# Optimization experiments

Hardware: AMD Instinct MI355X
Metric: run time of the kernel (lower is better)

The kernel has to match this reference:

```python
import jax, jax.numpy as jnp
import numpy as np

N_NODES = 50000
N_EDGES = 800000
IN_DIM = 128
HIDDEN = 64
NEG_SLOPE = 0.2


def setup_inputs() -> dict:
    key = jax.random.key(0)
    ks = jax.random.split(key, 8)
    x = jax.random.normal(ks[0], (N_NODES, IN_DIM), dtype=jnp.float32)
    edge_index = jax.random.randint(ks[1], (2, N_EDGES), 0, N_NODES, dtype=jnp.int64)
    # GATConv params (heads=1)
    W = jax.random.normal(ks[2], (HIDDEN, IN_DIM), dtype=jnp.float32) / np.sqrt(IN_DIM)
    att_src = jax.random.normal(ks[3], (HIDDEN,), dtype=jnp.float32) / np.sqrt(HIDDEN)
    att_dst = jax.random.normal(ks[4], (HIDDEN,), dtype=jnp.float32) / np.sqrt(HIDDEN)
    bias_conv = jnp.zeros((HIDDEN,), dtype=jnp.float32)
    # final Linear(hidden, 1)
    W_lin = jax.random.normal(ks[5], (1, HIDDEN), dtype=jnp.float32) / np.sqrt(HIDDEN)
    b_lin = jnp.zeros((1,), dtype=jnp.float32)
    return {"x": x, "edge_index": edge_index, "W": W, "att_src": att_src,
            "att_dst": att_dst, "bias_conv": bias_conv, "W_lin": W_lin, "b_lin": b_lin}


def _gat_forward(x, edge_index, W, att_src, att_dst, bias_conv, W_lin, b_lin):
    n = x.shape[0]
    # add self-loops (PyG GATConv default)
    loop = jnp.arange(n, dtype=edge_index.dtype)
    src = jnp.concatenate([edge_index[0], loop])  # source nodes j (messages from)
    dst = jnp.concatenate([edge_index[1], loop])  # destination nodes i (aggregated at)

    h = x @ W.T                                   # [N, H] projected features
    a_src = h @ att_src                           # [N]
    a_dst = h @ att_dst                           # [N]

    e = jax.nn.leaky_relu(a_src[src] + a_dst[dst], NEG_SLOPE)  # [E']
    # segment softmax over incoming edges of each destination node
    m = jax.ops.segment_max(e, dst, num_segments=n)            # [N]
    ex = jnp.exp(e - m[dst])
    s = jax.ops.segment_sum(ex, dst, num_segments=n)           # [N]
    alpha = ex / s[dst]                                        # [E']

    out = jax.ops.segment_sum(alpha[:, None] * h[src], dst, num_segments=n)
    out = out + bias_conv                         # [N, H]

    out = jax.nn.relu(out)
    # dropout p=0.5 is a no-op in eval mode
    y = jax.nn.sigmoid(out @ W_lin.T + b_lin)     # [N, 1]
    return y


def reference(x, edge_index, W, att_src, att_dst, bias_conv, W_lin, b_lin):
    return _gat_forward(x, edge_index, W, att_src, att_dst, bias_conv, W_lin, b_lin)
```

## Files before the change

### kernel.cpp

```cpp
#include <hip/hip_runtime.h>
#include <hip/hip_bf16.h>
#include <hip/hip_fp16.h>
#include <cstdint>

#define IND 128
#define HID 64
#define NEG_SLOPE 0.2f
#define EPB 4096
#define CBSHIFT 8
#define BCAP 8192
#define SORT_THREADS 256
#define EPT (EPB / SORT_THREADS)
#define QCAP 2048
#define GT 512
#define GSCAN (BCAP / GT)

__device__ __forceinline__ unsigned short f2bf_bits(float f) {
  __hip_bfloat16 b = __float2bfloat16(f);
  return *reinterpret_cast<unsigned short*>(&b);
}
__device__ __forceinline__ unsigned short f2h_bits(float f) {
  __half h = __float2half(f);
  return *reinterpret_cast<unsigned short*>(&h);
}
__device__ __forceinline__ float h2f_bits(unsigned short u) {
  __half_raw r; r.x = u;
  return __half2float(__half(r));
}
__device__ __forceinline__ float bf2f_bits(unsigned short u) {
  return __uint_as_float((unsigned)u << 16);
}
__device__ __forceinline__ unsigned pack_bf2(float lo, float hi) {
  return (unsigned)f2bf_bits(lo) | ((unsigned)f2bf_bits(hi) << 16);
}
__device__ __forceinline__ float bf_lo(unsigned u) {
  return __uint_as_float(u << 16);
}
__device__ __forceinline__ float bf_hi(unsigned u) {
  return __uint_as_float(u & 0xFFFF0000u);
}

__global__ __launch_bounds__(256) void k_proj_sort(
    const float* __restrict__ x, const float* __restrict__ W,
    const float* __restrict__ att_s, const float* __restrict__ att_d,
    unsigned short* __restrict__ h, float* __restrict__ a_src,
    float* __restrict__ a_dst,
    const int* __restrict__ ei, int* __restrict__ gcur,
    unsigned* __restrict__ tmp, int E, long long E2,
    int nSort, int nbuck, int n)
{
  __shared__ __align__(16) char smem[49664];
  const int tid = threadIdx.x;

  if (blockIdx.x < (unsigned)nSort) {
    int* hist       = (int*)smem;
    int* sums       = hist + 256;
    int* cur        = sums + 256;
    int* gbase      = cur + 256;
    unsigned* sorted = (unsigned*)(gbase + 256);

    hist[tid] = 0;
    __syncthreads();

    const long long i0 = (long long)blockIdx.x * EPB;

    unsigned pk[EPT];
#pragma unroll
    for (int j = 0; j < EPT; ++j) {
      long long idx = i0 + j * SORT_THREADS + tid;
      unsigned v = 0xFFFFFFFFu;
      if (idx < E2) {
        int s, d;
        if (idx < E) { s = ei[idx]; d = ei[E + idx]; }
        else         { s = d = (int)(idx - E); }
        v = ((unsigned)d << 16) | (unsigned)s;
        atomicAdd(&hist[d >> CBSHIFT], 1);
      }
      pk[j] = v;
    }
    __syncthreads();

    sums[tid] = hist[tid];
    __syncthreads();
    for (int off = 1; off < 256; off <<= 1) {
      int t = (tid >= off) ? sums[tid - off] : 0;
      __syncthreads();
      sums[tid] += t;
      __syncthreads();
    }
    {
      const int lstart_t = sums[tid] - hist[tid];
      cur[tid] = lstart_t;
      gbase[tid] = (tid < nbuck && hist[tid] > 0)
                     ? tid * BCAP + atomicAdd(&gcur[tid], hist[tid]) : 0;
    }
    __syncthreads();
    hist[tid] = sums[tid] - hist[tid];
    __syncthreads();

#pragma unroll
    for (int j = 0; j < EPT; ++j) {
      unsigned v = pk[j];
      if (v != 0xFFFFFFFFu) {
        int b = v >> (16 + CBSHIFT);
        int lpos = atomicAdd(&cur[b], 1);
        sorted[lpos] = v;
      }
    }
    __syncthreads();

    const int cntE = (int)((E2 - i0 < EPB) ? (E2 - i0) : EPB);
    for (int i = tid; i < cntE; i += SORT_THREADS) {
      unsigned v = sorted[i];
      int b = v >> (16 + CBSHIFT);
      tmp[gbase[b] + (i - hist[b])] = v;
    }
    return;
  }

  float*    xs   = (float*)smem;
  unsigned* wt   = (unsigned*)(smem + 32768);
  float*    sa_l = (float*)(smem + 49152);
  float*    sd_l = (float*)(smem + 49408);

  const int nodeBase = (blockIdx.x - nSort) * 64;

  if (tid < 64) { sa_l[tid] = 0.f; sd_l[tid] = 0.f; }

#pragma unroll
  for (int it = 0; it < 4; ++it) {
    int fi = (it * 256 + tid) * 8;
    int row = fi >> 7, k = fi & 127;
    float4 w0 = *(const float4*)(W + fi);
    float4 w1 = *(const float4*)(W + fi + 4);
    uint4 pv;
    pv.x = pack_bf2(w0.x, w0.y);
    pv.y = pack_bf2(w0.z, w0.w);
    pv.z = pack_bf2(w1.x, w1.y);
    pv.w = pack_bf2(w1.z, w1.w);
    int c = (k >> 3) ^ ((row >> 2) & 7);
    ((uint4*)wt)[row * 16 + c] = pv;
  }
#pragma unroll
  for (int it = 0; it < 8; ++it) {
    int fi = (it * 256 + tid) * 4;
    int nl = fi >> 7, k = fi & 127;
    int ks = k ^ (((nl >> 2) & 7) << 2);
    int node = nodeBase + nl; if (node >= n) node = n - 1;
    float4 v = *(const float4*)(x + (size_t)node * IND + k);
    *(float4*)&xs[nl * 128 + ks] = v;
  }
  __syncthreads();

  const int ng = tid & 15;
  const int hg = tid >> 4;
  const int swzA = (ng & 7) << 2;
  const int swzB = hg & 7;
  const float* xrow0 = &xs[(4 * ng) * 128];
  const uint4* wrow0 = ((const uint4*)wt) + (4 * hg) * 16;

  float acc[4][4];
#pragma unroll
  for (int j = 0; j < 4; ++j)
#pragma unroll
    for (int i = 0; i < 4; ++i) acc[j][i] = 0.f;

  for (int k = 0; k < IND; k += 8) {
    float4 a0[4], a1[4];
#pragma unroll
    for (int j = 0; j < 4; ++j) {
      a0[j] = *(const float4*)(xrow0 + j * 128 + (k ^ swzA));
      a1[j] = *(const float4*)(xrow0 + j * 128 + ((k + 4) ^ swzA));
    }
    uint4 bw[4];
#pragma unroll
    for (int i = 0; i < 4; ++i)
      bw[i] = wrow0[i * 16 + ((k >> 3) ^ swzB)];

#pragma unroll
    for (int i = 0; i < 4; ++i) {
      float b0 = bf_lo(bw[i].x), b1 = bf_hi(bw[i].x);
      float b2 = bf_lo(bw[i].y), b3 = bf_hi(bw[i].y);
      float b4 = bf_lo(bw[i].z), b5 = bf_hi(bw[i].z);
      float b6 = bf_lo(bw[i].w), b7 = bf_hi(bw[i].w);
#pragma unroll
      for (int j = 0; j < 4; ++j) {
        acc[j][i] = fmaf(a0[j].x, b0, acc[j][i]);
        acc[j][i] = fmaf(a0[j].y, b1, acc[j][i]);
        acc[j][i] = fmaf(a0[j].z, b2, acc[j][i]);
        acc[j][i] = fmaf(a0[j].w, b3, acc[j][i]);
        acc[j][i] = fmaf(a1[j].x, b4, acc[j][i]);
        acc[j][i] = fmaf(a1[j].y, b5, acc[j][i]);
        acc[j][i] = fmaf(a1[j].z, b6, acc[j][i]);
        acc[j][i] = fmaf(a1[j].w, b7, acc[j][i]);
      }
    }
  }

#pragma unroll
  for (int j = 0; j < 4; ++j) {
    int node = nodeBase + 4 * ng + j;
    if (node < n) {
      ushort4 hv;
      hv.x = f2bf_bits(acc[j][0]);
      hv.y = f2bf_bits(acc[j][1]);
      hv.z = f2bf_bits(acc[j][2]);
      hv.w = f2bf_bits(acc[j][3]);
      *(ushort4*)(h + (size_t)node * HID + 4 * hg) = hv;
    }
  }

  float4 as4 = *(const float4*)(att_s + 4 * hg);
  float4 ad4 = *(const float4*)(att_d + 4 * hg);
#pragma unroll
  for (int j = 0; j < 4; ++j) {
    float ps = acc[j][0]*as4.x + acc[j][1]*as4.y + acc[j][2]*as4.z + acc[j][3]*as4.w;
    float pd = acc[j][0]*ad4.x + acc[j][1]*ad4.y + acc[j][2]*ad4.z + acc[j][3]*ad4.w;
    ps += __shfl_xor(ps, 16, 64); ps += __shfl_xor(ps, 32, 64);
    pd += __shfl_xor(pd, 16, 64); pd += __shfl_xor(pd, 32, 64);
    if ((tid & 63) < 16) {
      atomicAdd(&sa_l[4 * ng + j], ps);
      atomicAdd(&sd_l[4 * ng + j], pd);
    }
  }
  __syncthreads();
  if (tid < 64) {
    int node = nodeBase + tid;
    if (node < n) { a_src[node] = sa_l[tid]; a_dst[node] = sd_l[tid]; }
  }
}

__global__ __launch_bounds__(GT) void k_csr_gather(
    const unsigned* __restrict__ tmp, const int* __restrict__ gcur,
    const float* __restrict__ a_src, const float* __restrict__ a_dst,
    const unsigned short* __restrict__ h,
    const float* __restrict__ bias, const float* __restrict__ W_lin,
    const float* __restrict__ b_lin, float* __restrict__ y, int n)
{
  __shared__ int degl[64], sums[64], cur[64];
  __shared__ float adl[64];
  __shared__ unsigned csrw[QCAP];

  const int tid  = threadIdx.x;
  const int blk  = blockIdx.x;
  const int b    = blk >> 2;
  const int n0   = (b << CBSHIFT) + ((blk & 3) << 6);
  const int base = b * BCAP;
  const int next = base + gcur[b];

  if (tid < 64) {
    degl[tid] = 0;
    const int node = n0 + tid;
    adl[tid] = (node < n) ? a_dst[node] : 0.f;
  }
  __syncthreads();

  unsigned pkv[GSCAN];
#pragma unroll
  for (int j = 0; j < GSCAN; ++j) {
    int i = base + j * GT + tid;
    unsigned v = 0xFFFFFFFFu;
    if (i < next) {
      v = tmp[i];
      unsigned dl = (v >> 16) - (unsigned)n0;
      if (dl < 64u) atomicAdd(&degl[dl], 1);
      else v = 0xFFFFFFFFu;
    }
    pkv[j] = v;
  }
  __syncthreads();

  if (tid == 0 && sums != nullptr) {}
  if (tid < 64) sums[tid] = degl[tid];
  __syncthreads();
  for (int off = 1; off < 64; off <<= 1) {
    int t = (tid >= off && tid < 64) ? sums[tid - off] : 0;
    __syncthreads();
    if (tid < 64) sums[tid] += t;
    __syncthreads();
  }
  if (tid < 64) cur[tid] = sums[tid] - degl[tid];
  __syncthreads();

#pragma unroll
  for (int j = 0; j < GSCAN; ++j) {
    unsigned v = pkv[j];
    if (v != 0xFFFFFFFFu) {
      unsigned dl = (v >> 16) - (unsigned)n0;
      int s = (int)(v & 0xFFFFu);
      float sc = a_src[s] + adl[dl];
      sc = (sc >= 0.f) ? sc : NEG_SLOPE * sc;
      float w = expf(sc);
      int pos = atomicAdd(&cur[dl], 1);
      if (pos < QCAP)
        csrw[pos] = (unsigned)s | ((unsigned)f2h_bits(w) << 16);
    }
  }
  __syncthreads();

  const int lane    = tid & 63;
  const int wid     = tid >> 6;
  const int quarter = lane >> 4;
  const int sub     = lane & 15;

  for (int nl = wid; nl < 64; nl += 8) {
    const int node = n0 + nl;
    if (node >= n) break;

    int rsl = sums[nl] - degl[nl];
    int dg  = degl[nl];
    if (rsl + dg > QCAP) dg = (QCAP > rsl) ? (QCAP - rsl) : 0;
    if (rsl >= QCAP) { rsl = 0; dg = 0; }

    float wpart = 0.f;
    float acc0 = 0.f, acc1 = 0.f, acc2 = 0.f, acc3 = 0.f;

    for (int bb = 0; bb < dg; bb += 64) {
      int i = bb + lane;
      unsigned pk = (i < dg) ? csrw[rsl + i] : 0u;
      wpart += h2f_bits((unsigned short)(pk >> 16));
      const int cnt = (dg - bb < 64) ? (dg - bb) : 64;

      int j = 0;
      for (; j + 8 <= cnt; j += 8) {
#pragma unroll
        for (int g = 0; g < 2; ++g) {
          int e = j + 4 * g + quarter;
          unsigned pe = __shfl(pk, e, 64);
          float we = h2f_bits((unsigned short)(pe >> 16));
          unsigned se = pe & 0xFFFFu;
          ushort4 hb = ((const ushort4*)(h + (size_t)se * HID))[sub];
          acc0 = fmaf(we, bf2f_bits(hb.x), acc0);
          acc1 = fmaf(we, bf2f_bits(hb.y), acc1);
          acc2 = fmaf(we, bf2f_bits(hb.z), acc2);
          acc3 = fmaf(we, bf2f_bits(hb.w), acc3);
        }
      }
      for (; j < cnt; j += 4) {
        int e = j + quarter;
        bool val = e < cnt;
        unsigned pe = __shfl(pk, val ? e : 0, 64);
        float we = val ? h2f_bits((unsigned short)(pe >> 16)) : 0.f;
        unsigned se = val ? (pe & 0xFFFFu) : 0u;
        ushort4 hb = ((const ushort4*)(h + (size_t)se * HID))[sub];
        acc0 = fmaf(we, bf2f_bits(hb.x), acc0);
        acc1 = fmaf(we, bf2f_bits(hb.y), acc1);
        acc2 = fmaf(we, bf2f_bits(hb.z), acc2);
        acc3 = fmaf(we, bf2f_bits(hb.w), acc3);
      }
    }

    acc0 += __shfl_xor(acc0, 16, 64); acc0 += __shfl_xor(acc0, 32, 64);
    acc1 += __shfl_xor(acc1, 16, 64); acc1 += __shfl_xor(acc1, 32, 64);
    acc2 += __shfl_xor(acc2, 16, 64); acc2 += __shfl_xor(acc2, 32, 64);
    acc3 += __shfl_xor(acc3, 16, 64); acc3 += __shfl_xor(acc3, 32, 64);

    float wsum = wpart;
#pragma unroll
    for (int o = 32; o; o >>= 1) wsum += __shfl_xor(wsum, o, 64);
    const float inv = 1.f / wsum;

    float4 bb4 = ((const float4*)bias)[sub];
    float4 ww  = ((const float4*)W_lin)[sub];
    float v0 = fmaxf(acc0 * inv + bb4.x, 0.f);
    float v1 = fmaxf(acc1 * inv + bb4.y, 0.f);
    float v2 = fmaxf(acc2 * inv + bb4.z, 0.f);
    float v3 = fmaxf(acc3 * inv + bb4.w, 0.f);
    float z = v0 * ww.x + v1 * ww.y + v2 * ww.z + v3 * ww.w;
#pragma unroll
    for (int o = 8; o; o >>= 1) z += __shfl_xor(z, o, 64);
    if (lane == 0)
      y[node] = 1.f / (1.f + expf(-(z + b_lin[0])));
  }
}


extern "C" void kernel_launch(void* const* d_in, const int* in_sizes, int n_in,
                              void* d_out, int out_size, void* d_ws, size_t ws_size,
                              hipStream_t stream)
{
  const float* x     = (const float*)d_in[0];
  const int*   ei    = (const int*)d_in[1];
  const float* W     = (const float*)d_in[2];
  const float* att_s = (const float*)d_in[3];
  const float* att_d = (const float*)d_in[4];
  const float* bias  = (const float*)d_in[5];
  const float* W_lin = (const float*)d_in[6];
  const float* b_lin = (const float*)d_in[7];
  float* y = (float*)d_out;

  const int n = in_sizes[0] / IND;
  const int E = in_sizes[1] / 2;
  const long long E2 = (long long)E + n;
  const int nSort = (int)((E2 + EPB - 1) / EPB);
  const int nProj = (n + 63) / 64;
  const int nbuck = (n + (1 << CBSHIFT) - 1) >> CBSHIFT;

  char* ws = (char*)d_ws;
  unsigned short* h = (unsigned short*)ws; ws += (size_t)n * HID * sizeof(unsigned short);
  float*    a_src  = (float*)ws;    ws += (size_t)n * sizeof(float);
  float*    a_dst  = (float*)ws;    ws += (size_t)n * sizeof(float);
  int*      gcur   = (int*)ws;      ws += (size_t)nbuck * sizeof(int);
  unsigned* tmp    = (unsigned*)ws; ws += (size_t)nbuck * BCAP * sizeof(unsigned);

  hipMemsetAsync(gcur, 0, (size_t)nbuck * sizeof(int), stream);

  k_proj_sort<<<nSort + nProj, 256, 0, stream>>>(
      x, W, att_s, att_d, h, a_src, a_dst,
      ei, gcur, tmp, E, E2, nSort, nbuck, n);

  k_csr_gather<<<nbuck * 4, GT, 0, stream>>>(
      tmp, gcur, a_src, a_dst, h, bias, W_lin, b_lin, y, n);
}
```

Measured before the change: 136.8 us.

## Compute node projection with bf16 MFMA instead of scalar FMA

Replaces the shared-memory-tiled fp32 FMA projection (x staged in LDS, bf16 W) with MFMA 16x16x32 bf16 instructions. x rows are loaded straight from global memory into registers and converted to bf16 fragments, which removes the x LDS staging and shrinks shared memory from about 49 KB to 20 KB, so more blocks can be resident. The attention dot products are now reduced with in-wave shuffles instead of LDS atomics. In exchange, x is rounded to bf16, which lowers precision. The h stores are now scalar 2-byte writes rather than vectorised ones.

```diff
diff --git a/kernel.cpp b/kernel.cpp
--- a/kernel.cpp
+++ b/kernel.cpp
@@ -15,6 +15,9 @@
 #define GT 512
 #define GSCAN (BCAP / GT)
 
+typedef __attribute__((ext_vector_type(8))) short bf16x8;
+typedef __attribute__((ext_vector_type(4))) float f32x4;
+
 __device__ __forceinline__ unsigned short f2bf_bits(float f) {
   __hip_bfloat16 b = __float2bfloat16(f);
   return *reinterpret_cast<unsigned short*>(&b);
@@ -33,11 +36,16 @@
 __device__ __forceinline__ unsigned pack_bf2(float lo, float hi) {
   return (unsigned)f2bf_bits(lo) | ((unsigned)f2bf_bits(hi) << 16);
 }
-__device__ __forceinline__ float bf_lo(unsigned u) {
-  return __uint_as_float(u << 16);
-}
-__device__ __forceinline__ float bf_hi(unsigned u) {
-  return __uint_as_float(u & 0xFFFF0000u);
+__device__ __forceinline__ bf16x8 mk_bf16x8(unsigned a, unsigned b,
+                                            unsigned c, unsigned d) {
+  union { unsigned u[4]; bf16x8 v; } t;
+  t.u[0] = a; t.u[1] = b; t.u[2] = c; t.u[3] = d;
+  return t.v;
+}
+__device__ __forceinline__ bf16x8 mk_bf16x8_u4(uint4 u) {
+  union { uint4 u4; bf16x8 v; } t;
+  t.u4 = u;
+  return t.v;
 }
 
 __global__ __launch_bounds__(256) void k_proj_sort(
@@ -49,7 +57,7 @@
     unsigned* __restrict__ tmp, int E, long long E2,
     int nSort, int nbuck, int n)
 {
-  __shared__ __align__(16) char smem[49664];
+  __shared__ __align__(16) char smem[20480];
   const int tid = threadIdx.x;
 
   if (blockIdx.x < (unsigned)nSort) {
@@ -118,14 +126,9 @@
     return;
   }
 
-  float*    xs   = (float*)smem;
-  unsigned* wt   = (unsigned*)(smem + 32768);
-  float*    sa_l = (float*)(smem + 49152);
-  float*    sd_l = (float*)(smem + 49408);
+  unsigned* wt = (unsigned*)smem;
 
   const int nodeBase = (blockIdx.x - nSort) * 64;
-
-  if (tid < 64) { sa_l[tid] = 0.f; sd_l[tid] = 0.f; }
 
 #pragma unroll
   for (int it = 0; it < 4; ++it) {
@@ -141,92 +144,78 @@
     int c = (k >> 3) ^ ((row >> 2) & 7);
     ((uint4*)wt)[row * 16 + c] = pv;
   }
-#pragma unroll
-  for (int it = 0; it < 8; ++it) {
-    int fi = (it * 256 + tid) * 4;
-    int nl = fi >> 7, k = fi & 127;
-    int ks = k ^ (((nl >> 2) & 7) << 2);
-    int node = nodeBase + nl; if (node >= n) node = n - 1;
-    float4 v = *(const float4*)(x + (size_t)node * IND + k);
-    *(float4*)&xs[nl * 128 + ks] = v;
-  }
-  __syncthreads();
-
-  const int ng = tid & 15;
-  const int hg = tid >> 4;
-  const int swzA = (ng & 7) << 2;
-  const int swzB = hg & 7;
-  const float* xrow0 = &xs[(4 * ng) * 128];
-  const uint4* wrow0 = ((const uint4*)wt) + (4 * hg) * 16;
-
-  float acc[4][4];
-#pragma unroll
-  for (int j = 0; j < 4; ++j)
-#pragma unroll
-    for (int i = 0; i < 4; ++i) acc[j][i] = 0.f;
-
-  for (int k = 0; k < IND; k += 8) {
-    float4 a0[4], a1[4];
-#pragma unroll
-    for (int j = 0; j < 4; ++j) {
-      a0[j] = *(const float4*)(xrow0 + j * 128 + (k ^ swzA));
-      a1[j] = *(const float4*)(xrow0 + j * 128 + ((k + 4) ^ swzA));
-    }
-    uint4 bw[4];
-#pragma unroll
-    for (int i = 0; i < 4; ++i)
-      bw[i] = wrow0[i * 16 + ((k >> 3) ^ swzB)];
-
-#pragma unroll
-    for (int i = 0; i < 4; ++i) {
-      float b0 = bf_lo(bw[i].x), b1 = bf_hi(bw[i].x);
-      float b2 = bf_lo(bw[i].y), b3 = bf_hi(bw[i].y);
-      float b4 = bf_lo(bw[i].z), b5 = bf_hi(bw[i].z);
-      float b6 = bf_lo(bw[i].w), b7 = bf_hi(bw[i].w);
-#pragma unroll
-      for (int j = 0; j < 4; ++j) {
-        acc[j][i] = fmaf(a0[j].x, b0, acc[j][i]);
-        acc[j][i] = fmaf(a0[j].y, b1, acc[j][i]);
-        acc[j][i] = fmaf(a0[j].z, b2, acc[j][i]);
-        acc[j][i] = fmaf(a0[j].w, b3, acc[j][i]);
-        acc[j][i] = fmaf(a1[j].x, b4, acc[j][i]);
-        acc[j][i] = fmaf(a1[j].y, b5, acc[j][i]);
-        acc[j][i] = fmaf(a1[j].z, b6, acc[j][i]);
-        acc[j][i] = fmaf(a1[j].w, b7, acc[j][i]);
-      }
-    }
-  }
-
-#pragma unroll
-  for (int j = 0; j < 4; ++j) {
-    int node = nodeBase + 4 * ng + j;
-    if (node < n) {
-      ushort4 hv;
-      hv.x = f2bf_bits(acc[j][0]);
-      hv.y = f2bf_bits(acc[j][1]);
-      hv.z = f2bf_bits(acc[j][2]);
-      hv.w = f2bf_bits(acc[j][3]);
-      *(ushort4*)(h + (size_t)node * HID + 4 * hg) = hv;
-    }
-  }
-
-  float4 as4 = *(const float4*)(att_s + 4 * hg);
-  float4 ad4 = *(const float4*)(att_d + 4 * hg);
-#pragma unroll
-  for (int j = 0; j < 4; ++j) {
-    float ps = acc[j][0]*as4.x + acc[j][1]*as4.y + acc[j][2]*as4.z + acc[j][3]*as4.w;
-    float pd = acc[j][0]*ad4.x + acc[j][1]*ad4.y + acc[j][2]*ad4.z + acc[j][3]*ad4.w;
-    ps += __shfl_xor(ps, 16, 64); ps += __shfl_xor(ps, 32, 64);
-    pd += __shfl_xor(pd, 16, 64); pd += __shfl_xor(pd, 32, 64);
-    if ((tid & 63) < 16) {
-      atomicAdd(&sa_l[4 * ng + j], ps);
-      atomicAdd(&sd_l[4 * ng + j], pd);
-    }
-  }
-  __syncthreads();
-  if (tid < 64) {
-    int node = nodeBase + tid;
-    if (node < n) { a_src[node] = sa_l[tid]; a_dst[node] = sd_l[tid]; }
+  __syncthreads();
+
+  const int lane = tid & 63;
+  const int wid4 = tid >> 6;
+  const int r16  = lane & 15;
+  const int q    = lane >> 4;
+
+  const int arow = nodeBase + 16 * wid4 + r16;
+  const size_t xoff = (size_t)((arow < n) ? arow : (n - 1)) * IND;
+
+  float4 xv[8];
+#pragma unroll
+  for (int ks = 0; ks < 4; ++ks) {
+    xv[2 * ks]     = *(const float4*)(x + xoff + 32 * ks + 8 * q);
+    xv[2 * ks + 1] = *(const float4*)(x + xoff + 32 * ks + 8 * q + 4);
+  }
+
+  f32x4 acc0 = {0.f, 0.f, 0.f, 0.f};
+  f32x4 acc1 = {0.f, 0.f, 0.f, 0.f};
+  f32x4 acc2 = {0.f, 0.f, 0.f, 0.f};
+  f32x4 acc3 = {0.f, 0.f, 0.f, 0.f};
+
+#pragma unroll
+  for (int ks = 0; ks < 4; ++ks) {
+    float4 xa = xv[2 * ks], xb = xv[2 * ks + 1];
+    bf16x8 afrag = mk_bf16x8(pack_bf2(xa.x, xa.y), pack_bf2(xa.z, xa.w),
+                             pack_bf2(xb.x, xb.y), pack_bf2(xb.z, xb.w));
+    {
+      int row = r16;
+      uint4 bw = ((const uint4*)wt)[row * 16 + ((4 * ks + q) ^ ((row >> 2) & 7))];
+      acc0 = __builtin_amdgcn_mfma_f32_16x16x32_bf16(afrag, mk_bf16x8_u4(bw), acc0, 0, 0, 0);
+    }
+    {
+      int row = 16 + r16;
+      uint4 bw = ((const uint4*)wt)[row * 16 + ((4 * ks + q) ^ ((row >> 2) & 7))];
+      acc1 = __builtin_amdgcn_mfma_f32_16x16x32_bf16(afrag, mk_bf16x8_u4(bw), acc1, 0, 0, 0);
+    }
+    {
+      int row = 32 + r16;
+      uint4 bw = ((const uint4*)wt)[row * 16 + ((4 * ks + q) ^ ((row >> 2) & 7))];
+      acc2 = __builtin_amdgcn_mfma_f32_16x16x32_bf16(afrag, mk_bf16x8_u4(bw), acc2, 0, 0, 0);
+    }
+    {
+      int row = 48 + r16;
+      uint4 bw = ((const uint4*)wt)[row * 16 + ((4 * ks + q) ^ ((row >> 2) & 7))];
+      acc3 = __builtin_amdgcn_mfma_f32_16x16x32_bf16(afrag, mk_bf16x8_u4(bw), acc3, 0, 0, 0);
+    }
+  }
+
+  const float as0 = att_s[r16],      ad0 = att_d[r16];
+  const float as1 = att_s[16 + r16], ad1 = att_d[16 + r16];
+  const float as2 = att_s[32 + r16], ad2 = att_d[32 + r16];
+  const float as3 = att_s[48 + r16], ad3 = att_d[48 + r16];
+
+#pragma unroll
+  for (int reg = 0; reg < 4; ++reg) {
+    const int node = nodeBase + 16 * wid4 + 4 * q + reg;
+    const bool ok = (node < n);
+    if (ok) {
+      const size_t hb = (size_t)node * HID;
+      h[hb + r16]      = f2bf_bits(acc0[reg]);
+      h[hb + 16 + r16] = f2bf_bits(acc1[reg]);
+      h[hb + 32 + r16] = f2bf_bits(acc2[reg]);
+      h[hb + 48 + r16] = f2bf_bits(acc3[reg]);
+    }
+    float ps = acc0[reg] * as0 + acc1[reg] * as1 + acc2[reg] * as2 + acc3[reg] * as3;
+    float pd = acc0[reg] * ad0 + acc1[reg] * ad1 + acc2[reg] * ad2 + acc3[reg] * ad3;
+    ps += __shfl_xor(ps, 1, 64); ps += __shfl_xor(ps, 2, 64);
+    ps += __shfl_xor(ps, 4, 64); ps += __shfl_xor(ps, 8, 64);
+    pd += __shfl_xor(pd, 1, 64); pd += __shfl_xor(pd, 2, 64);
+    pd += __shfl_xor(pd, 4, 64); pd += __shfl_xor(pd, 8, 64);
+    if (ok && r16 == 0) { a_src[node] = ps; a_dst[node] = pd; }
   }
 }
 
@@ -270,7 +259,6 @@
   }
   __syncthreads();
 
-  if (tid == 0 && sums != nullptr) {}
   if (tid < 64) sums[tid] = degl[tid];
   __syncthreads();
   for (int off = 1; off < 64; off <<= 1) {
```

After: 129.9 us. -5.0%, faster.
